# Optimization experiments

Measured on AMD Instinct MI355X. Metric: run time of the kernel, lower is better.

Reference implementation:

```python
import jax, jax.numpy as jnp
import numpy as np

D_MODEL = 1024
NUM_HEADS = 16
ROPE_THETA = 10000.0
NEG_INF = -1.0e9  # matches torch masked_fill value


def _rope(x, cos, sin):
    # x: (B, H, S, d_k); cos/sin: (1, 1, S, d_k) with interleaved-pair layout
    x_even = x[..., ::2]
    x_odd = x[..., 1::2]
    x_rot = jnp.stack((-x_odd, x_even), axis=-1).reshape(x.shape)
    return x * cos + x_rot * sin


def setup_inputs() -> dict:
    key = jax.random.key(0)
    ks = jax.random.split(key, 5)
    B, S, D = 2, 2048, D_MODEL
    std = np.sqrt(2.0 / (D + D))
    return {
        "x": jax.random.normal(ks[0], (B, S, D), dtype=jnp.float32),
        "token_positions": jnp.arange(S, dtype=jnp.int32)[None, :],
        "Wq": jax.random.normal(ks[1], (D, D), dtype=jnp.float32) * std,
        "Wk": jax.random.normal(ks[2], (D, D), dtype=jnp.float32) * std,
        "Wv": jax.random.normal(ks[3], (D, D), dtype=jnp.float32) * std,
        "Wo": jax.random.normal(ks[4], (D, D), dtype=jnp.float32) * std,
    }


def reference(x, token_positions, Wq, Wk, Wv, Wo):
    B, S, D = x.shape
    H = NUM_HEADS
    dk = D // H

    def proj(W):
        return (x @ W.T).reshape(B, S, H, dk).transpose(0, 2, 1, 3)  # (B,H,S,dk)

    q, k, v = proj(Wq), proj(Wk), proj(Wv)

    # RoPE tables (interleaved repeat of each frequency)
    inv_freq = 1.0 / ROPE_THETA ** (jnp.arange(0, dk, 2, dtype=jnp.float32) / dk)
    angles = token_positions.astype(jnp.float32)[..., None] * inv_freq  # (1,S,dk/2)
    angles = jnp.repeat(angles, 2, axis=-1)  # (1,S,dk)
    cos = jnp.cos(angles)[:, None, :, :]  # (1,1,S,dk)
    sin = jnp.sin(angles)[:, None, :, :]
    q = _rope(q, cos, sin)
    k = _rope(k, cos, sin)

    scores = jnp.einsum("bhqd,bhkd->bhqk", q, k) / jnp.sqrt(jnp.float32(dk))
    causal = jnp.tril(jnp.ones((S, S), dtype=bool))
    scores = jnp.where(causal, scores, NEG_INF)
    attn = jax.nn.softmax(scores, axis=-1)
    out = jnp.einsum("bhqk,bhkd->bhqd", attn, v)
    out = out.transpose(0, 2, 1, 3).reshape(B, S, D)
    return out @ Wo.T
```

## Files before the change

kernel.cpp:

```cpp
#include <hip/hip_runtime.h>
#include <hip/hip_bf16.h>
#include <stdint.h>

typedef __bf16 bf16_t;
typedef __attribute__((ext_vector_type(8))) __bf16 bf16x8;
typedef __attribute__((ext_vector_type(4))) __bf16 bf16x4;
typedef __attribute__((ext_vector_type(2))) __bf16 bf16x2;
typedef __attribute__((ext_vector_type(4))) float f32x4;
typedef __attribute__((ext_vector_type(16))) float f32x16;
typedef __attribute__((ext_vector_type(4))) uint32_t u32x4;

#define S_LEN 2048
#define DMODEL 1024
#define NHEAD 16
#define DK 64
#define TENS_ELEMS 4194304

__device__ __forceinline__ void async_load16(const bf16_t* g, bf16_t* l) {
  __builtin_amdgcn_global_load_lds(
      (const __attribute__((address_space(1))) uint32_t*)(const void*)g,
      (__attribute__((address_space(3))) uint32_t*)(void*)l,
      16, 0, 0);
}

__device__ __forceinline__ uint32_t pack_bf16(float a, float b) {
  bf16x2 h; h[0] = (bf16_t)a; h[1] = (bf16_t)b;
  return __builtin_bit_cast(uint32_t, h);
}

__global__ __launch_bounds__(256) void cvt_kernel(const float* __restrict__ src,
                                                  bf16_t* __restrict__ dst, int n4) {
  int i = blockIdx.x * 256 + threadIdx.x;
  if (i >= n4) return;
  float4 v = ((const float4*)src)[i];
  bf16x4 o;
  o.x = (bf16_t)v.x; o.y = (bf16_t)v.y; o.z = (bf16_t)v.z; o.w = (bf16_t)v.w;
  ((bf16x4*)dst)[i] = o;
}

__global__ __launch_bounds__(256) void cvt4_kernel(const float* __restrict__ s0,
                                                   const float* __restrict__ s1,
                                                   const float* __restrict__ s2,
                                                   const float* __restrict__ s3,
                                                   bf16_t* __restrict__ dst) {
  int i = blockIdx.x * 256 + threadIdx.x;
  int y = blockIdx.y;
  const float* s = (y == 0) ? s0 : (y == 1) ? s1 : (y == 2) ? s2 : s3;
  float4 v = ((const float4*)s)[i];
  bf16x4 o;
  o.x = (bf16_t)v.x; o.y = (bf16_t)v.y; o.z = (bf16_t)v.z; o.w = (bf16_t)v.w;
  ((bf16x4*)(dst + (size_t)y * 1048576))[i] = o;
}

__global__ __launch_bounds__(256) void rope_kernel(bf16_t* __restrict__ Q,
                                                   bf16_t* __restrict__ K,
                                                   const int* __restrict__ tok) {
  int idx = blockIdx.x * 256 + threadIdx.x;
  bf16_t* T = blockIdx.y ? K : Q;
  int i  = idx & 31;
  int s  = (idx >> 5) & 2047;
  int bh = idx >> 16;
  float p   = (float)tok[s];
  float inv = __expf(-(float)i * 0.28782313662425572f);
  float sn, cs;
  sincosf(p * inv, &sn, &cs);
  bf16_t* ptr = T + ((size_t)bh * S_LEN + s) * DK + 2 * i;
  float e = (float)ptr[0], o = (float)ptr[1];
  ptr[0] = (bf16_t)(e * cs - o * sn);
  ptr[1] = (bf16_t)(o * cs + e * sn);
}

template <int MODE>
__global__ __launch_bounds__(256) void gemm_nt(const bf16_t* __restrict__ A,
                                               const bf16_t* __restrict__ Bw,
                                               bf16_t* __restrict__ Cb,
                                               float* __restrict__ Cf) {
  __shared__ bf16_t As[64 * 64];
  __shared__ bf16_t Bs[128 * 64];
  const int K = 1024;
  int tid = threadIdx.x;
  int lane = tid & 63, w = tid >> 6, lo = lane & 15, hi = lane >> 4;
  int m0 = blockIdx.y * 64, n0 = blockIdx.x * 128;
  const bf16_t* Bp = Bw + (size_t)blockIdx.z * 1048576;
  f32x4 acc[4][2] = {};
  for (int k0 = 0; k0 < K; k0 += 64) {
#pragma unroll
    for (int it = 0; it < 2; ++it) {
      int idx = it * 256 + tid;
      int row = idx >> 3, kc = (idx & 7) * 8;
      async_load16(A + (size_t)(m0 + row) * K + k0 + kc, &As[idx * 8]);
    }
#pragma unroll
    for (int it = 0; it < 4; ++it) {
      int idx = it * 256 + tid;
      int row = idx >> 3, kc = (idx & 7) * 8;
      async_load16(Bp + (size_t)(n0 + row) * K + k0 + kc, &Bs[idx * 8]);
    }
    __syncthreads();
#pragma unroll
    for (int ks = 0; ks < 2; ++ks) {
      bf16x8 af[4], bfr[2];
#pragma unroll
      for (int mi = 0; mi < 4; ++mi)
        af[mi] = *(const bf16x8*)&As[(mi * 16 + lo) * 64 + ks * 32 + hi * 8];
#pragma unroll
      for (int ni = 0; ni < 2; ++ni)
        bfr[ni] = *(const bf16x8*)&Bs[(w * 32 + ni * 16 + lo) * 64 + ks * 32 + hi * 8];
#pragma unroll
      for (int mi = 0; mi < 4; ++mi)
#pragma unroll
        for (int ni = 0; ni < 2; ++ni)
          acc[mi][ni] = __builtin_amdgcn_mfma_f32_16x16x32_bf16(af[mi], bfr[ni], acc[mi][ni], 0, 0, 0);
    }
    __syncthreads();
  }
#pragma unroll
  for (int mi = 0; mi < 4; ++mi) {
#pragma unroll
    for (int ni = 0; ni < 2; ++ni) {
      int col = n0 + w * 32 + ni * 16 + lo;
      int rb = m0 + mi * 16 + hi * 4;
      if (MODE == 0) {
        int h = col >> 6, d = col & 63;
        if (blockIdx.z == 2) {
          bf16_t* Vt = Cb + 3 * (size_t)TENS_ELEMS;
          int b = rb >> 11, s = rb & 2047;
          int bh2 = b * NHEAD + h;
          bf16x4 ov;
#pragma unroll
          for (int r = 0; r < 4; ++r) ov[r] = (bf16_t)acc[mi][ni][r];
          *(bf16x4*)(Vt + (((size_t)(bh2 * 32 + (s >> 6)) * 64 + d) * 64 + (s & 63))) = ov;
        } else {
          bf16_t* C = Cb + (size_t)blockIdx.z * TENS_ELEMS;
#pragma unroll
          for (int r = 0; r < 4; ++r) {
            int row = rb + r;
            int b = row >> 11, s = row & 2047;
            C[(((size_t)(b * NHEAD + h)) * S_LEN + s) * DK + d] = (bf16_t)acc[mi][ni][r];
          }
        }
      } else {
#pragma unroll
        for (int r = 0; r < 4; ++r) {
          int row = rb + r;
          Cf[(size_t)row * 1024 + col] = acc[mi][ni][r];
        }
      }
    }
  }
}

__global__ __launch_bounds__(256, 2) void attn_kernel(const bf16_t* __restrict__ Q,
                                                      const bf16_t* __restrict__ K,
                                                      const bf16_t* __restrict__ Vt,
                                                      bf16_t* __restrict__ O) {
  __shared__ float S_lds[3][32][66];
  int tid = threadIdx.x;
  int w = tid >> 6, lane = tid & 63;
  int lq = lane & 31, hi = lane >> 5;
  int g = blockIdx.x;
  int bh = (g & 7) * 4 + (g >> 8);
  int qp = (g >> 3) & 31;

  const bf16_t* Kb = K + (size_t)bh * S_LEN * DK;
  const bf16_t* Vb = Vt + (size_t)bh * DK * S_LEN;
  const bf16_t* kp = Kb + (size_t)lq * DK + hi * 8;
  int b_out = bh >> 4, h_out = bh & 15;

  for (int ph = 0; ph < 2; ++ph) {
    int qt = ph ? (63 - qp) : qp;
    int q0 = qt * 32;

    const bf16_t* Qp = Q + ((size_t)bh * S_LEN + q0 + lq) * DK + hi * 8;
    bf16x8 qf[4];
#pragma unroll
    for (int ks = 0; ks < 4; ++ks) qf[ks] = *(const bf16x8*)(Qp + ks * 16);

    f32x16 oa0 = {}, oa1 = {};
    float m = -1e30f, lsum = 0.f;

    int nT = (q0 + 95) >> 6;
    int tB = (nT * w) >> 2, tE = (nT * (w + 1)) >> 2;

    for (int t = tB; t < tE; ++t) {
      int kv0 = t * 64;
      bf16x8 kc[8];
      const bf16_t* kpt = kp + (size_t)kv0 * DK;
#pragma unroll
      for (int i = 0; i < 8; ++i)
        kc[i] = *(const bf16x8*)(kpt + (size_t)(i >> 2) * 32 * DK + (i & 3) * 16);
      bf16x8 vf[8];
      const bf16_t* vtile = Vb + (size_t)t * 4096 + 8 * hi;
#pragma unroll
      for (int sub = 0; sub < 2; ++sub)
#pragma unroll
        for (int u = 0; u < 4; ++u)
          vf[sub * 4 + u] = *(const bf16x8*)(vtile + (32 * sub + lq) * 64 + 16 * u);
      f32x16 s0 = {}, s1 = {};
#pragma unroll
      for (int ks = 0; ks < 4; ++ks)
        s0 = __builtin_amdgcn_mfma_f32_32x32x16_bf16(kc[ks], qf[ks], s0, 0, 0, 0);
#pragma unroll
      for (int ks = 0; ks < 4; ++ks)
        s1 = __builtin_amdgcn_mfma_f32_32x32x16_bf16(kc[4 + ks], qf[ks], s1, 0, 0, 0);
      float p[32];
      bool needMask = (kv0 + 63 > q0);
#pragma unroll
      for (int r = 0; r < 16; ++r) {
        float v0 = s0[r] * 0.125f, v1 = s1[r] * 0.125f;
        if (needMask) {
          int kvr = kv0 + (r & 3) + 8 * (r >> 2) + 4 * hi;
          if (kvr > q0 + lq) v0 = -1e9f;
          if (kvr + 32 > q0 + lq) v1 = -1e9f;
        }
        p[r] = v0; p[16 + r] = v1;
      }
      float tm[16];
#pragma unroll
      for (int i = 0; i < 16; ++i) tm[i] = fmaxf(p[i], p[16 + i]);
#pragma unroll
      for (int i = 0; i < 8; ++i) tm[i] = fmaxf(tm[i], tm[8 + i]);
#pragma unroll
      for (int i = 0; i < 4; ++i) tm[i] = fmaxf(tm[i], tm[4 + i]);
      float mt = fmaxf(fmaxf(tm[0], tm[1]), fmaxf(tm[2], tm[3]));
      mt = fmaxf(mt, __shfl_xor(mt, 32));
      if (__any(mt > m)) {
        float mn = fmaxf(m, mt);
        float a = __expf(m - mn);
        m = mn;
        lsum *= a;
#pragma unroll
        for (int r = 0; r < 16; ++r) { oa0[r] *= a; oa1[r] *= a; }
      }
      float ts[16];
#pragma unroll
      for (int i = 0; i < 32; ++i) p[i] = __expf(p[i] - m);
#pragma unroll
      for (int i = 0; i < 16; ++i) ts[i] = p[i] + p[16 + i];
#pragma unroll
      for (int i = 0; i < 8; ++i) ts[i] += ts[8 + i];
#pragma unroll
      for (int i = 0; i < 4; ++i) ts[i] += ts[4 + i];
      float sum = (ts[0] + ts[1]) + (ts[2] + ts[3]);
      sum += __shfl_xor(sum, 32);
      lsum += sum;
      uint32_t pk[16], xk[16];
#pragma unroll
      for (int c = 0; c < 16; ++c) pk[c] = pack_bf16(p[2 * c], p[2 * c + 1]);
#pragma unroll
      for (int c = 0; c < 16; ++c) xk[c] = (uint32_t)__shfl_xor((int)pk[c], 32);
#pragma unroll
      for (int tt = 0; tt < 2; ++tt)
#pragma unroll
        for (int j = 0; j < 2; ++j) {
          int c0 = 8 * tt + 4 * j;
          uint32_t b0 = hi ? xk[c0 + 2] : pk[c0];
          uint32_t b1 = hi ? xk[c0 + 3] : pk[c0 + 1];
          uint32_t b2 = hi ? pk[c0 + 2] : xk[c0];
          uint32_t b3 = hi ? pk[c0 + 3] : xk[c0 + 1];
          u32x4 bb = {b0, b1, b2, b3};
          bf16x8 pb = __builtin_bit_cast(bf16x8, bb);
          int u = 2 * tt + j;
          oa0 = __builtin_amdgcn_mfma_f32_32x32x16_bf16(vf[u], pb, oa0, 0, 0, 0);
          oa1 = __builtin_amdgcn_mfma_f32_32x32x16_bf16(vf[4 + u], pb, oa1, 0, 0, 0);
        }
    }

    if (w > 0) {
      float* Sp = &S_lds[w - 1][lq][0];
#pragma unroll
      for (int g2 = 0; g2 < 4; ++g2)
#pragma unroll
        for (int i = 0; i < 4; ++i) {
          Sp[8 * g2 + 4 * hi + i]      = oa0[4 * g2 + i];
          Sp[32 + 8 * g2 + 4 * hi + i] = oa1[4 * g2 + i];
        }
      if (hi == 0) { Sp[64] = m; Sp[65] = lsum; }
    }
    __syncthreads();
    if (w == 0) {
      float mp0 = S_lds[0][lq][64], lp0 = S_lds[0][lq][65];
      float mp1 = S_lds[1][lq][64], lp1 = S_lds[1][lq][65];
      float mp2 = S_lds[2][lq][64], lp2 = S_lds[2][lq][65];
      float M = fmaxf(fmaxf(m, mp0), fmaxf(mp1, mp2));
      float w0 = __expf(m - M),  w1 = __expf(mp0 - M);
      float w2 = __expf(mp1 - M), w3 = __expf(mp2 - M);
      float lc = lsum * w0 + lp0 * w1 + lp1 * w2 + lp2 * w3;
      float inv = 1.0f / lc;
      bf16_t* Op = O + ((size_t)(b_out * S_LEN + q0 + lq)) * DMODEL + h_out * 64;
#pragma unroll
      for (int g2 = 0; g2 < 4; ++g2) {
        bf16x4 ov0, ov1;
#pragma unroll
        for (int i = 0; i < 4; ++i) {
          int c0 = 8 * g2 + 4 * hi + i;
          float v0 = oa0[4 * g2 + i] * w0 + S_lds[0][lq][c0] * w1
                   + S_lds[1][lq][c0] * w2 + S_lds[2][lq][c0] * w3;
          float v1 = oa1[4 * g2 + i] * w0 + S_lds[0][lq][32 + c0] * w1
                   + S_lds[1][lq][32 + c0] * w2 + S_lds[2][lq][32 + c0] * w3;
          ov0[i] = (bf16_t)(v0 * inv);
          ov1[i] = (bf16_t)(v1 * inv);
        }
        *(bf16x4*)(Op + 8 * g2 + 4 * hi) = ov0;
        *(bf16x4*)(Op + 32 + 8 * g2 + 4 * hi) = ov1;
      }
    }
    __syncthreads();
  }
}

extern "C" void kernel_launch(void* const* d_in, const int* in_sizes, int n_in,
                              void* d_out, int out_size, void* d_ws, size_t ws_size,
                              hipStream_t stream) {
  const float* x  = (const float*)d_in[0];
  const int* tok  = (const int*)d_in[1];
  const float* Wq = (const float*)d_in[2];
  const float* Wk = (const float*)d_in[3];
  const float* Wv = (const float*)d_in[4];
  const float* Wo = (const float*)d_in[5];
  float* out = (float*)d_out;

  bf16_t* xb  = (bf16_t*)d_ws;
  bf16_t* Wb  = xb + TENS_ELEMS;
  bf16_t* Qb  = Wb + TENS_ELEMS;
  bf16_t* Kb  = Qb + TENS_ELEMS;
  bf16_t* Vb  = Kb + TENS_ELEMS;
  bf16_t* Vtb = Vb + TENS_ELEMS;
  bf16_t* Ab  = Vtb + TENS_ELEMS;

  cvt_kernel<<<4096, 256, 0, stream>>>(x, xb, 1048576);
  cvt4_kernel<<<dim3(1024, 4), 256, 0, stream>>>(Wq, Wk, Wv, Wo, Wb);

  gemm_nt<0><<<dim3(8, 64, 3), 256, 0, stream>>>(xb, Wb, Qb, nullptr);
  rope_kernel<<<dim3(8192, 2), 256, 0, stream>>>(Qb, Kb, tok);
  attn_kernel<<<1024, 256, 0, stream>>>(Qb, Kb, Vtb, Ab);
  gemm_nt<1><<<dim3(8, 64, 1), 256, 0, stream>>>(Ab, Wb + 3145728, nullptr, out);
}
```

Baseline: 164.0 us.

## Merge conversion kernels, fold softmax scale into RoPE, prefetch next K tile

The two fp32-to-bf16 conversion launches become one kernel covering x and all four weights, saving a launch. The 1/sqrt(dk) scale is applied to Q inside the RoPE kernel instead of to every score in the attention loop, removing per-element multiplies. The attention loop now loads the next K tile into registers while softmax runs on the current one, hiding global-load latency. This raises register pressure, and rounding Q to bf16 after scaling changes numerics slightly.

```diff
diff --git a/kernel.cpp b/kernel.cpp
--- a/kernel.cpp
+++ b/kernel.cpp
@@ -28,28 +28,29 @@
   return __builtin_bit_cast(uint32_t, h);
 }
 
-__global__ __launch_bounds__(256) void cvt_kernel(const float* __restrict__ src,
-                                                  bf16_t* __restrict__ dst, int n4) {
-  int i = blockIdx.x * 256 + threadIdx.x;
-  if (i >= n4) return;
-  float4 v = ((const float4*)src)[i];
-  bf16x4 o;
-  o.x = (bf16_t)v.x; o.y = (bf16_t)v.y; o.z = (bf16_t)v.z; o.w = (bf16_t)v.w;
-  ((bf16x4*)dst)[i] = o;
-}
-
-__global__ __launch_bounds__(256) void cvt4_kernel(const float* __restrict__ s0,
-                                                   const float* __restrict__ s1,
-                                                   const float* __restrict__ s2,
-                                                   const float* __restrict__ s3,
-                                                   bf16_t* __restrict__ dst) {
-  int i = blockIdx.x * 256 + threadIdx.x;
-  int y = blockIdx.y;
-  const float* s = (y == 0) ? s0 : (y == 1) ? s1 : (y == 2) ? s2 : s3;
+__global__ __launch_bounds__(256) void cvt_all(const float* __restrict__ x,
+                                               const float* __restrict__ w0,
+                                               const float* __restrict__ w1,
+                                               const float* __restrict__ w2,
+                                               const float* __restrict__ w3,
+                                               bf16_t* __restrict__ xb,
+                                               bf16_t* __restrict__ wb) {
+  int b = blockIdx.x;
+  const float* s;
+  bf16_t* d;
+  int i;
+  if (b < 4096) {
+    s = x; d = xb; i = b * 256 + threadIdx.x;
+  } else {
+    int k = (b - 4096) >> 10, j = (b - 4096) & 1023;
+    s = (k == 0) ? w0 : (k == 1) ? w1 : (k == 2) ? w2 : w3;
+    d = wb + (size_t)k * 1048576;
+    i = j * 256 + threadIdx.x;
+  }
   float4 v = ((const float4*)s)[i];
   bf16x4 o;
   o.x = (bf16_t)v.x; o.y = (bf16_t)v.y; o.z = (bf16_t)v.z; o.w = (bf16_t)v.w;
-  ((bf16x4*)(dst + (size_t)y * 1048576))[i] = o;
+  ((bf16x4*)d)[i] = o;
 }
 
 __global__ __launch_bounds__(256) void rope_kernel(bf16_t* __restrict__ Q,
@@ -57,6 +58,7 @@
                                                    const int* __restrict__ tok) {
   int idx = blockIdx.x * 256 + threadIdx.x;
   bf16_t* T = blockIdx.y ? K : Q;
+  float sc = blockIdx.y ? 1.0f : 0.125f;
   int i  = idx & 31;
   int s  = (idx >> 5) & 2047;
   int bh = idx >> 16;
@@ -66,8 +68,8 @@
   sincosf(p * inv, &sn, &cs);
   bf16_t* ptr = T + ((size_t)bh * S_LEN + s) * DK + 2 * i;
   float e = (float)ptr[0], o = (float)ptr[1];
-  ptr[0] = (bf16_t)(e * cs - o * sn);
-  ptr[1] = (bf16_t)(o * cs + e * sn);
+  ptr[0] = (bf16_t)((e * cs - o * sn) * sc);
+  ptr[1] = (bf16_t)((o * cs + e * sn) * sc);
 }
 
 template <int MODE>
@@ -182,88 +184,103 @@
     int nT = (q0 + 95) >> 6;
     int tB = (nT * w) >> 2, tE = (nT * (w + 1)) >> 2;
 
-    for (int t = tB; t < tE; ++t) {
-      int kv0 = t * 64;
+    if (tB < tE) {
       bf16x8 kc[8];
-      const bf16_t* kpt = kp + (size_t)kv0 * DK;
+      const bf16_t* kp0 = kp + (size_t)(tB * 64) * DK;
 #pragma unroll
       for (int i = 0; i < 8; ++i)
-        kc[i] = *(const bf16x8*)(kpt + (size_t)(i >> 2) * 32 * DK + (i & 3) * 16);
-      bf16x8 vf[8];
-      const bf16_t* vtile = Vb + (size_t)t * 4096 + 8 * hi;
-#pragma unroll
-      for (int sub = 0; sub < 2; ++sub)
-#pragma unroll
-        for (int u = 0; u < 4; ++u)
-          vf[sub * 4 + u] = *(const bf16x8*)(vtile + (32 * sub + lq) * 64 + 16 * u);
-      f32x16 s0 = {}, s1 = {};
-#pragma unroll
-      for (int ks = 0; ks < 4; ++ks)
-        s0 = __builtin_amdgcn_mfma_f32_32x32x16_bf16(kc[ks], qf[ks], s0, 0, 0, 0);
-#pragma unroll
-      for (int ks = 0; ks < 4; ++ks)
-        s1 = __builtin_amdgcn_mfma_f32_32x32x16_bf16(kc[4 + ks], qf[ks], s1, 0, 0, 0);
-      float p[32];
-      bool needMask = (kv0 + 63 > q0);
-#pragma unroll
-      for (int r = 0; r < 16; ++r) {
-        float v0 = s0[r] * 0.125f, v1 = s1[r] * 0.125f;
-        if (needMask) {
-          int kvr = kv0 + (r & 3) + 8 * (r >> 2) + 4 * hi;
-          if (kvr > q0 + lq) v0 = -1e9f;
-          if (kvr + 32 > q0 + lq) v1 = -1e9f;
-        }
-        p[r] = v0; p[16 + r] = v1;
+        kc[i] = *(const bf16x8*)(kp0 + (size_t)(i >> 2) * 32 * DK + (i & 3) * 16);
+
+      for (int t = tB; t < tE; ++t) {
+        int kv0 = t * 64;
+        bf16x8 vf[8];
+        const bf16_t* vtile = Vb + (size_t)t * 4096 + 8 * hi;
+#pragma unroll
+        for (int sub = 0; sub < 2; ++sub)
+#pragma unroll
+          for (int u = 0; u < 4; ++u)
+            vf[sub * 4 + u] = *(const bf16x8*)(vtile + (32 * sub + lq) * 64 + 16 * u);
+        f32x16 s0 = {}, s1 = {};
+#pragma unroll
+        for (int ks = 0; ks < 4; ++ks)
+          s0 = __builtin_amdgcn_mfma_f32_32x32x16_bf16(kc[ks], qf[ks], s0, 0, 0, 0);
+#pragma unroll
+        for (int ks = 0; ks < 4; ++ks)
+          s1 = __builtin_amdgcn_mfma_f32_32x32x16_bf16(kc[4 + ks], qf[ks], s1, 0, 0, 0);
+        bf16x8 kn[8];
+        bool more = (t + 1 < tE);
+        if (more) {
+          const bf16_t* kpn = kp + (size_t)(kv0 + 64) * DK;
+#pragma unroll
+          for (int i = 0; i < 8; ++i)
+            kn[i] = *(const bf16x8*)(kpn + (size_t)(i >> 2) * 32 * DK + (i & 3) * 16);
+        }
+        float p[32];
+        bool needMask = (kv0 + 63 > q0);
+#pragma unroll
+        for (int r = 0; r < 16; ++r) {
+          float v0 = s0[r], v1 = s1[r];
+          if (needMask) {
+            int kvr = kv0 + (r & 3) + 8 * (r >> 2) + 4 * hi;
+            if (kvr > q0 + lq) v0 = -1e9f;
+            if (kvr + 32 > q0 + lq) v1 = -1e9f;
+          }
+          p[r] = v0; p[16 + r] = v1;
+        }
+        float tm[16];
+#pragma unroll
+        for (int i = 0; i < 16; ++i) tm[i] = fmaxf(p[i], p[16 + i]);
+#pragma unroll
+        for (int i = 0; i < 8; ++i) tm[i] = fmaxf(tm[i], tm[8 + i]);
+#pragma unroll
+        for (int i = 0; i < 4; ++i) tm[i] = fmaxf(tm[i], tm[4 + i]);
+        float mt = fmaxf(fmaxf(tm[0], tm[1]), fmaxf(tm[2], tm[3]));
+        mt = fmaxf(mt, __shfl_xor(mt, 32));
+        if (__any(mt > m)) {
+          float mn = fmaxf(m, mt);
+          float a = __expf(m - mn);
+          m = mn;
+          lsum *= a;
+#pragma unroll
+          for (int r = 0; r < 16; ++r) { oa0[r] *= a; oa1[r] *= a; }
+        }
+        float ts[16];
+#pragma unroll
+        for (int i = 0; i < 32; ++i) p[i] = __expf(p[i] - m);
+#pragma unroll
+        for (int i = 0; i < 16; ++i) ts[i] = p[i] + p[16 + i];
+#pragma unroll
+        for (int i = 0; i < 8; ++i) ts[i] += ts[8 + i];
+#pragma unroll
+        for (int i = 0; i < 4; ++i) ts[i] += ts[4 + i];
+        float sum = (ts[0] + ts[1]) + (ts[2] + ts[3]);
+        sum += __shfl_xor(sum, 32);
+        lsum += sum;
+        uint32_t pk[16], xk[16];
+#pragma unroll
+        for (int c = 0; c < 16; ++c) pk[c] = pack_bf16(p[2 * c], p[2 * c + 1]);
+#pragma unroll
+        for (int c = 0; c < 16; ++c) xk[c] = (uint32_t)__shfl_xor((int)pk[c], 32);
+#pragma unroll
+        for (int tt = 0; tt < 2; ++tt)
+#pragma unroll
+          for (int j = 0; j < 2; ++j) {
+            int c0 = 8 * tt + 4 * j;
+            uint32_t b0 = hi ? xk[c0 + 2] : pk[c0];
+            uint32_t b1 = hi ? xk[c0 + 3] : pk[c0 + 1];
+            uint32_t b2 = hi ? pk[c0 + 2] : xk[c0];
+            uint32_t b3 = hi ? pk[c0 + 3] : xk[c0 + 1];
+            u32x4 bb = {b0, b1, b2, b3};
+            bf16x8 pb = __builtin_bit_cast(bf16x8, bb);
+            int u = 2 * tt + j;
+            oa0 = __builtin_amdgcn_mfma_f32_32x32x16_bf16(vf[u], pb, oa0, 0, 0, 0);
+            oa1 = __builtin_amdgcn_mfma_f32_32x32x16_bf16(vf[4 + u], pb, oa1, 0, 0, 0);
+          }
+        if (more) {
+#pragma unroll
+          for (int i = 0; i < 8; ++i) kc[i] = kn[i];
+        }
       }
-      float tm[16];
-#pragma unroll
-      for (int i = 0; i < 16; ++i) tm[i] = fmaxf(p[i], p[16 + i]);
-#pragma unroll
-      for (int i = 0; i < 8; ++i) tm[i] = fmaxf(tm[i], tm[8 + i]);
-#pragma unroll
-      for (int i = 0; i < 4; ++i) tm[i] = fmaxf(tm[i], tm[4 + i]);
-      float mt = fmaxf(fmaxf(tm[0], tm[1]), fmaxf(tm[2], tm[3]));
-      mt = fmaxf(mt, __shfl_xor(mt, 32));
-      if (__any(mt > m)) {
-        float mn = fmaxf(m, mt);
-        float a = __expf(m - mn);
-        m = mn;
-        lsum *= a;
-#pragma unroll
-        for (int r = 0; r < 16; ++r) { oa0[r] *= a; oa1[r] *= a; }
-      }
-      float ts[16];
-#pragma unroll
-      for (int i = 0; i < 32; ++i) p[i] = __expf(p[i] - m);
-#pragma unroll
-      for (int i = 0; i < 16; ++i) ts[i] = p[i] + p[16 + i];
-#pragma unroll
-      for (int i = 0; i < 8; ++i) ts[i] += ts[8 + i];
-#pragma unroll
-      for (int i = 0; i < 4; ++i) ts[i] += ts[4 + i];
-      float sum = (ts[0] + ts[1]) + (ts[2] + ts[3]);
-      sum += __shfl_xor(sum, 32);
-      lsum += sum;
-      uint32_t pk[16], xk[16];
-#pragma unroll
-      for (int c = 0; c < 16; ++c) pk[c] = pack_bf16(p[2 * c], p[2 * c + 1]);
-#pragma unroll
-      for (int c = 0; c < 16; ++c) xk[c] = (uint32_t)__shfl_xor((int)pk[c], 32);
-#pragma unroll
-      for (int tt = 0; tt < 2; ++tt)
-#pragma unroll
-        for (int j = 0; j < 2; ++j) {
-          int c0 = 8 * tt + 4 * j;
-          uint32_t b0 = hi ? xk[c0 + 2] : pk[c0];
-          uint32_t b1 = hi ? xk[c0 + 3] : pk[c0 + 1];
-          uint32_t b2 = hi ? pk[c0 + 2] : xk[c0];
-          uint32_t b3 = hi ? pk[c0 + 3] : xk[c0 + 1];
-          u32x4 bb = {b0, b1, b2, b3};
-          bf16x8 pb = __builtin_bit_cast(bf16x8, bb);
-          int u = 2 * tt + j;
-          oa0 = __builtin_amdgcn_mfma_f32_32x32x16_bf16(vf[u], pb, oa0, 0, 0, 0);
-          oa1 = __builtin_amdgcn_mfma_f32_32x32x16_bf16(vf[4 + u], pb, oa1, 0, 0, 0);
-        }
     }
 
     if (w > 0) {
@@ -328,8 +345,7 @@
   bf16_t* Vtb = Vb + TENS_ELEMS;
   bf16_t* Ab  = Vtb + TENS_ELEMS;
 
-  cvt_kernel<<<4096, 256, 0, stream>>>(x, xb, 1048576);
-  cvt4_kernel<<<dim3(1024, 4), 256, 0, stream>>>(Wq, Wk, Wv, Wo, Wb);
+  cvt_all<<<8192, 256, 0, stream>>>(x, Wq, Wk, Wv, Wo, xb, Wb);
 
   gemm_nt<0><<<dim3(8, 64, 3), 256, 0, stream>>>(xb, Wb, Qb, nullptr);
   rope_kernel<<<dim3(8192, 2), 256, 0, stream>>>(Qb, Kb, tok);
```

After: 162.0 us. Within noise of the previous version (-1.2%).
